# Kernel tuning notes

Hardware: AMD Instinct MI355X
Metric: run time of the kernel (lower is better)

The kernel has to match this reference:

```python
import jax, jax.numpy as jnp
import numpy as np

N = 10000      # nodes
E = 320000     # edges (avg degree 32)
IN = 512       # in_channels
OUT = 128      # out_channels
H = 4          # in_head
C1 = 2 * OUT   # per-head hidden channels of conv1 (256)
NEG_SLOPE = 0.2


def setup_inputs() -> dict:
    key = jax.random.key(0)
    ks = jax.random.split(key, 12)
    x = jax.random.normal(ks[0], (N, IN), dtype=jnp.float32)
    edge_index = jax.random.randint(ks[1], (2, E), 0, N, dtype=jnp.int64)
    def glorot(k, shape):
        lim = np.sqrt(6.0 / (shape[0] + shape[-1])).astype(np.float32)
        return jax.random.uniform(k, shape, jnp.float32, -lim, lim)
    # conv1: GATv2Conv(IN -> C1 per head, heads=H)
    Wl1 = glorot(ks[2], (IN, H * C1))
    Wr1 = glorot(ks[3], (IN, H * C1))
    att1 = glorot(ks[4], (H, C1))
    b1 = jnp.zeros((H * C1,), jnp.float32)
    # conv2: GATv2Conv(H*C1 -> OUT, heads=1)
    Wl2 = glorot(ks[5], (H * C1, OUT))
    Wr2 = glorot(ks[6], (H * C1, OUT))
    att2 = glorot(ks[7], (1, OUT))
    b2 = jnp.zeros((OUT,), jnp.float32)
    return {"x": x, "edge_index": edge_index, "Wl1": Wl1, "Wr1": Wr1,
            "att1": att1, "b1": b1, "Wl2": Wl2, "Wr2": Wr2,
            "att2": att2, "b2": b2}


def gatv2_conv(x, src, dst, Wl, Wr, att, b, heads, ch):
    # x: [N, F_in]; src/dst: [E] (message src -> dst, softmax over dst)
    n = x.shape[0]
    xl = (x @ Wl).reshape(n, heads, ch)   # source-side projection
    xr = (x @ Wr).reshape(n, heads, ch)   # target-side projection
    # per-edge GATv2 score: att . LeakyReLU(xl_j + xr_i)   [E, H]
    e = jax.nn.leaky_relu(xl[src] + xr[dst], NEG_SLOPE)    # [E, H, C]
    s = jnp.einsum('ehc,hc->eh', e, att)                   # [E, H]
    # segment softmax over incoming edges of each dst node
    smax = jax.lax.stop_gradient(jax.ops.segment_max(s, dst, num_segments=n))
    ex = jnp.exp(s - smax[dst])
    denom = jax.ops.segment_sum(ex, dst, num_segments=n)
    alpha = ex / denom[dst]                                # [E, H]
    # weighted scatter-add of source messages
    out = jax.ops.segment_sum(alpha[:, :, None] * xl[src], dst, num_segments=n)
    return out.reshape(n, heads * ch) + b                  # concat heads + bias


def reference(x, edge_index, Wl1, Wr1, att1, b1, Wl2, Wr2, att2, b2):
    src, dst = edge_index[0], edge_index[1]
    h = gatv2_conv(x, src, dst, Wl1, Wr1, att1, b1, H, C1)
    h = jax.nn.relu(h)                                     # [N, H*C1]
    out = gatv2_conv(h, src, dst, Wl2, Wr2, att2, b2, 1, OUT)
    return out                                             # [N, OUT]
```

## Files before the change

kernel.cpp:

```cpp
#include <hip/hip_runtime.h>
#include <cfloat>

#define N_NODES 10000
#define N_EDGES 320000
#define IN_F    512
#define F1      1024
#define OUT_F   128
#define NEG     0.2f
#define BUCKET  128

typedef __attribute__((ext_vector_type(8))) short bf16x8;
typedef __attribute__((ext_vector_type(4))) float f32x4;

__device__ __forceinline__ float lrelu(float v) { return fmaxf(v, NEG * v); }

__device__ __forceinline__ unsigned short f2bf(float f) {
    unsigned u = __float_as_uint(f);
    u += 0x7fff + ((u >> 16) & 1);
    return (unsigned short)(u >> 16);
}
__device__ __forceinline__ float bf2f(unsigned short h) {
    return __uint_as_float(((unsigned)h) << 16);
}
__device__ __forceinline__ void u2f2(unsigned u, float& e0, float& e1) {
    e0 = __uint_as_float(u << 16);
    e1 = __uint_as_float(u & 0xffff0000u);
}

__device__ __forceinline__ float rsum16(float x) {
    x += __int_as_float(__builtin_amdgcn_update_dpp(0, __float_as_int(x), 0x121, 0xF, 0xF, false));
    x += __int_as_float(__builtin_amdgcn_update_dpp(0, __float_as_int(x), 0x122, 0xF, 0xF, false));
    x += __int_as_float(__builtin_amdgcn_update_dpp(0, __float_as_int(x), 0x124, 0xF, 0xF, false));
    x += __int_as_float(__builtin_amdgcn_update_dpp(0, __float_as_int(x), 0x128, 0xF, 0xF, false));
    return x;
}

__device__ __forceinline__ void gld_lds16(const void* g, void* l) {
    __builtin_amdgcn_global_load_lds(
        (const __attribute__((address_space(1))) unsigned int*)g,
        (__attribute__((address_space(3))) unsigned int*)l, 16, 0, 0);
}

#define PB_X  2500
#define PB_S  3750
#define PB_W1 4774
#define PB_END 5030

__device__ __forceinline__ void wt_body(const float* __restrict__ Wa,
                                        const float* __restrict__ Wb,
                                        unsigned short* __restrict__ tbf,
                                        int K, int NS, int n0, int k0, int t,
                                        float (*tile)[33]) {
    int j = t & 31;
    const float* W = (n0 < NS) ? Wa : Wb;
    int nb = (n0 < NS) ? n0 : n0 - NS;
#pragma unroll
    for (int r = 0; r < 4; ++r) {
        int kl = (t >> 5) + r * 8;
        tile[kl][j] = W[(size_t)(k0 + kl) * NS + nb + j];
    }
    __syncthreads();
#pragma unroll
    for (int r = 0; r < 4; ++r) {
        int nl = (t >> 5) + r * 8;
        tbf[(size_t)(n0 + nl) * K + k0 + j] = f2bf(tile[j][nl]);
    }
}

__global__ __launch_bounds__(256) void k_prep(const float* __restrict__ x,
                                              unsigned short* __restrict__ xbf,
                                              const int* __restrict__ ei,
                                              int* __restrict__ cnt,
                                              int* __restrict__ esrc,
                                              const float* __restrict__ Wl1,
                                              const float* __restrict__ Wr1,
                                              unsigned short* __restrict__ w1bf,
                                              const float* __restrict__ Wl2,
                                              const float* __restrict__ Wr2,
                                              unsigned short* __restrict__ w2bf) {
    __shared__ float tile[32][33];
    int bid = blockIdx.x, t = threadIdx.x;
    if (bid < PB_X) {
        int i = bid * 2048 + t * 8;
        float4 v0 = *(const float4*)(x + i);
        float4 v1 = *(const float4*)(x + i + 4);
        ushort4 h0, h1;
        h0.x = f2bf(v0.x); h0.y = f2bf(v0.y); h0.z = f2bf(v0.z); h0.w = f2bf(v0.w);
        h1.x = f2bf(v1.x); h1.y = f2bf(v1.y); h1.z = f2bf(v1.z); h1.w = f2bf(v1.w);
        *(ushort4*)(xbf + i) = h0;
        *(ushort4*)(xbf + i + 4) = h1;
    } else if (bid < PB_S) {
        int e = (bid - PB_X) * 256 + t;
        if (e < N_EDGES) {
            int d = ei[N_EDGES + e];
            int pos = atomicAdd(&cnt[d], 1);
            if (pos < BUCKET) esrc[(size_t)d * BUCKET + pos] = ei[e];
        }
    } else if (bid < PB_W1) {
        int local = bid - PB_S;
        wt_body(Wl1, Wr1, w1bf, IN_F, F1, (local & 63) * 32, (local >> 6) * 32, t, tile);
    } else {
        int local = bid - PB_W1;
        wt_body(Wl2, Wr2, w2bf, F1, OUT_F, (local & 7) * 32, (local >> 3) * 32, t, tile);
    }
}

template<int BM, int WR, int WC>
__global__ __launch_bounds__(256) void gemm_mfma(
        const unsigned short* __restrict__ A,
        const unsigned short* __restrict__ B,
        unsigned short* __restrict__ Cl, unsigned short* __restrict__ Cr,
        int M, int K, int NSPLIT) {
    constexpr int NI = BM / (16 * WR);
    constexpr int NJ = 128 / (16 * WC);
    __shared__ __align__(16) short As[BM * 32];
    __shared__ __align__(16) short Bs[128 * 32];
    int t = threadIdx.x;
    int lane = t & 63, w = t >> 6;
    int row0 = blockIdx.y * BM;
    int n0 = blockIdx.x * 128;
    int wr0 = (w / WC) * (NI * 16);
    int wc0 = (w % WC) * (NJ * 16);
    int q = lane >> 4, md = lane & 15;
    int srow = t >> 2;
    int skoff = (t & 3) * 8;

    f32x4 acc[NI][NJ];
#pragma unroll
    for (int i = 0; i < NI; ++i)
#pragma unroll
        for (int j = 0; j < NJ; ++j)
#pragma unroll
            for (int r = 0; r < 4; ++r) acc[i][j][r] = 0.f;

    for (int k0 = 0; k0 < K; k0 += 32) {
        __syncthreads();
#pragma unroll
        for (int is = 0; is < BM / 64; ++is) {
            int gr = row0 + is * 64 + srow;
            if (gr < M)
                gld_lds16(A + (size_t)gr * K + k0 + skoff,
                          &As[(is * 64 + (t >> 6) * 16) * 32]);
        }
#pragma unroll
        for (int is = 0; is < 2; ++is) {
            int gn = n0 + is * 64 + srow;
            gld_lds16(B + (size_t)gn * K + k0 + skoff,
                      &Bs[(is * 64 + (t >> 6) * 16) * 32]);
        }
        __syncthreads();

        bf16x8 av[NI], bv[NJ];
#pragma unroll
        for (int i = 0; i < NI; ++i)
            av[i] = *(const bf16x8*)&As[(wr0 + i * 16 + md) * 32 + q * 8];
#pragma unroll
        for (int j = 0; j < NJ; ++j)
            bv[j] = *(const bf16x8*)&Bs[(wc0 + j * 16 + md) * 32 + q * 8];
#pragma unroll
        for (int i = 0; i < NI; ++i)
#pragma unroll
            for (int j = 0; j < NJ; ++j)
                acc[i][j] = __builtin_amdgcn_mfma_f32_16x16x32_bf16(av[i], bv[j], acc[i][j], 0, 0, 0);
    }

#pragma unroll
    for (int i = 0; i < NI; ++i)
#pragma unroll
        for (int j = 0; j < NJ; ++j) {
            int col = n0 + wc0 + j * 16 + md;
            unsigned short* C = (col < NSPLIT) ? Cl : Cr;
            int cc = (col < NSPLIT) ? col : col - NSPLIT;
#pragma unroll
            for (int r = 0; r < 4; ++r) {
                int grow = row0 + wr0 + i * 16 + q * 4 + r;
                if (grow < M) C[(size_t)grow * NSPLIT + cc] = f2bf(acc[i][j][r]);
            }
        }
}

__global__ __launch_bounds__(256) void k_pq1(const unsigned short* __restrict__ xlbf,
                                             const float* __restrict__ att,
                                             float* __restrict__ P) {
    int t = threadIdx.x;
    int w = t >> 6, lane = t & 63;
    int nd = blockIdx.x * 4 + w;
    int head = lane >> 4, sub = lane & 15;
    int ch = head * 256 + sub * 16;
    const uint4* px = (const uint4*)(xlbf + (size_t)nd * F1 + ch);
    uint4 xa = px[0], xb = px[1];
    const float4* pa = (const float4*)(att + ch);
    float4 a0 = pa[0], a1 = pa[1], a2 = pa[2], a3 = pa[3];
    float4 c0, c1, c2, c3;
    u2f2(xa.x, c0.x, c0.y); u2f2(xa.y, c0.z, c0.w);
    u2f2(xa.z, c1.x, c1.y); u2f2(xa.w, c1.z, c1.w);
    u2f2(xb.x, c2.x, c2.y); u2f2(xb.y, c2.z, c2.w);
    u2f2(xb.z, c3.x, c3.y); u2f2(xb.w, c3.z, c3.w);
    float s0 = a0.x * c0.x;
    s0 = fmaf(a0.y, c0.y, s0); s0 = fmaf(a0.z, c0.z, s0); s0 = fmaf(a0.w, c0.w, s0);
    float s1 = a1.x * c1.x;
    s1 = fmaf(a1.y, c1.y, s1); s1 = fmaf(a1.z, c1.z, s1); s1 = fmaf(a1.w, c1.w, s1);
    float s2 = a2.x * c2.x;
    s2 = fmaf(a2.y, c2.y, s2); s2 = fmaf(a2.z, c2.z, s2); s2 = fmaf(a2.w, c2.w, s2);
    float s3 = a3.x * c3.x;
    s3 = fmaf(a3.y, c3.y, s3); s3 = fmaf(a3.z, c3.z, s3); s3 = fmaf(a3.w, c3.w, s3);
    float s = rsum16((s0 + s1) + (s2 + s3));
    if (sub == 0) P[nd * 4 + head] = s;
}

__global__ __launch_bounds__(256) void k_fused1(const unsigned short* __restrict__ xlbf,
                                                const unsigned short* __restrict__ xrbf,
                                                const int* __restrict__ cnt,
                                                const int* __restrict__ esrc,
                                                const float* __restrict__ att,
                                                const float* __restrict__ Pbuf,
                                                const float* __restrict__ bias,
                                                unsigned short* __restrict__ hb) {
    int t = threadIdx.x;
    int w = t >> 6, lane = t & 63;
    int nd = blockIdx.x * 4 + w;
    int head = lane >> 4, sub = lane & 15;
    int ch = head * 256 + sub * 16;

    float4 r0, r1, r2, r3;
    {
        const uint4* prx = (const uint4*)(xrbf + (size_t)nd * F1 + ch);
        uint4 xa = prx[0], xb = prx[1];
        u2f2(xa.x, r0.x, r0.y); u2f2(xa.y, r0.z, r0.w);
        u2f2(xa.z, r1.x, r1.y); u2f2(xa.w, r1.z, r1.w);
        u2f2(xb.x, r2.x, r2.y); u2f2(xb.y, r2.z, r2.w);
        u2f2(xb.z, r3.x, r3.y); u2f2(xb.w, r3.z, r3.w);
    }
    const float4* pa = (const float4*)(att + ch);
    float4 a0 = pa[0], a1 = pa[1], a2 = pa[2], a3 = pa[3];

    float qd = a0.x * r0.x;
    qd = fmaf(a0.y, r0.y, qd); qd = fmaf(a0.z, r0.z, qd); qd = fmaf(a0.w, r0.w, qd);
    qd = fmaf(a1.x, r1.x, qd); qd = fmaf(a1.y, r1.y, qd);
    qd = fmaf(a1.z, r1.z, qd); qd = fmaf(a1.w, r1.w, qd);
    qd = fmaf(a2.x, r2.x, qd); qd = fmaf(a2.y, r2.y, qd);
    qd = fmaf(a2.z, r2.z, qd); qd = fmaf(a2.w, r2.w, qd);
    qd = fmaf(a3.x, r3.x, qd); qd = fmaf(a3.y, r3.y, qd);
    qd = fmaf(a3.z, r3.z, qd); qd = fmaf(a3.w, r3.w, qd);
    float Qk = 0.6f * rsum16(qd);

    int deg = min(cnt[nd], BUCKET);
    int p0 = nd * BUCKET;
    int p1 = p0 + deg;

    float l = 0.f;
    float4 acc0 = make_float4(0.f, 0.f, 0.f, 0.f);
    float4 acc1 = acc0, acc2 = acc0, acc3 = acc0;

    uint4 A0 = {}, B0 = {}, A1 = {}, B1 = {};
    float Pv0 = 0.f, Pv1 = 0.f;
    if (p0 < p1) {
        int sn = esrc[p0];
        const uint4* pv = (const uint4*)(xlbf + (size_t)sn * F1 + ch);
        A0 = pv[0]; B0 = pv[1]; Pv0 = Pbuf[sn * 4 + head];
    }
    if (p0 + 1 < p1) {
        int sn = esrc[p0 + 1];
        const uint4* pv = (const uint4*)(xlbf + (size_t)sn * F1 + ch);
        A1 = pv[0]; B1 = pv[1]; Pv1 = Pbuf[sn * 4 + head];
    }
    for (int p = p0; p < p1; ++p) {
        uint4 ca = A0, cb = B0;
        float Pv = Pv0;
        A0 = A1; B0 = B1; Pv0 = Pv1;
        if (p + 2 < p1) {
            int sn = esrc[p + 2];
            const uint4* pv = (const uint4*)(xlbf + (size_t)sn * F1 + ch);
            A1 = pv[0]; B1 = pv[1]; Pv1 = Pbuf[sn * 4 + head];
        }
        float4 c0, c1, c2, c3;
        u2f2(ca.x, c0.x, c0.y); u2f2(ca.y, c0.z, c0.w);
        u2f2(ca.z, c1.x, c1.y); u2f2(ca.w, c1.z, c1.w);
        u2f2(cb.x, c2.x, c2.y); u2f2(cb.y, c2.z, c2.w);
        u2f2(cb.z, c3.x, c3.y); u2f2(cb.w, c3.z, c3.w);
        float s0 = a0.x * fabsf(c0.x + r0.x);
        s0 = fmaf(a0.y, fabsf(c0.y + r0.y), s0);
        s0 = fmaf(a0.z, fabsf(c0.z + r0.z), s0);
        s0 = fmaf(a0.w, fabsf(c0.w + r0.w), s0);
        float s1 = a1.x * fabsf(c1.x + r1.x);
        s1 = fmaf(a1.y, fabsf(c1.y + r1.y), s1);
        s1 = fmaf(a1.z, fabsf(c1.z + r1.z), s1);
        s1 = fmaf(a1.w, fabsf(c1.w + r1.w), s1);
        float s2 = a2.x * fabsf(c2.x + r2.x);
        s2 = fmaf(a2.y, fabsf(c2.y + r2.y), s2);
        s2 = fmaf(a2.z, fabsf(c2.z + r2.z), s2);
        s2 = fmaf(a2.w, fabsf(c2.w + r2.w), s2);
        float s3 = a3.x * fabsf(c3.x + r3.x);
        s3 = fmaf(a3.y, fabsf(c3.y + r3.y), s3);
        s3 = fmaf(a3.z, fabsf(c3.z + r3.z), s3);
        s3 = fmaf(a3.w, fabsf(c3.w + r3.w), s3);
        float sab = rsum16((s0 + s1) + (s2 + s3));
        float sarg = fmaf(0.6f, Pv, Qk);
        sarg = fmaf(0.4f, sab, sarg);
        sarg = fminf(fmaxf(sarg, -60.f), 60.f);
        float al = __expf(sarg);
        l += al;
        acc0.x = fmaf(al, c0.x, acc0.x);
        acc0.y = fmaf(al, c0.y, acc0.y);
        acc0.z = fmaf(al, c0.z, acc0.z);
        acc0.w = fmaf(al, c0.w, acc0.w);
        acc1.x = fmaf(al, c1.x, acc1.x);
        acc1.y = fmaf(al, c1.y, acc1.y);
        acc1.z = fmaf(al, c1.z, acc1.z);
        acc1.w = fmaf(al, c1.w, acc1.w);
        acc2.x = fmaf(al, c2.x, acc2.x);
        acc2.y = fmaf(al, c2.y, acc2.y);
        acc2.z = fmaf(al, c2.z, acc2.z);
        acc2.w = fmaf(al, c2.w, acc2.w);
        acc3.x = fmaf(al, c3.x, acc3.x);
        acc3.y = fmaf(al, c3.y, acc3.y);
        acc3.z = fmaf(al, c3.z, acc3.z);
        acc3.w = fmaf(al, c3.w, acc3.w);
    }

    float invL = (l > 0.f) ? 1.f / l : 0.f;
    const float4* pb = (const float4*)(bias + ch);
    size_t base = (size_t)nd * F1 + ch;
    float4 aa[4] = {acc0, acc1, acc2, acc3};
#pragma unroll
    for (int j = 0; j < 4; ++j) {
        float4 b4 = pb[j];
        ushort4 hv;
        hv.x = f2bf(fmaxf(fmaf(aa[j].x, invL, b4.x), 0.f));
        hv.y = f2bf(fmaxf(fmaf(aa[j].y, invL, b4.y), 0.f));
        hv.z = f2bf(fmaxf(fmaf(aa[j].z, invL, b4.z), 0.f));
        hv.w = f2bf(fmaxf(fmaf(aa[j].w, invL, b4.w), 0.f));
        *(ushort4*)(hb + base + j * 4) = hv;
    }
}

__global__ __launch_bounds__(256) void k_fused2(const unsigned short* __restrict__ xlbf,
                                                const unsigned short* __restrict__ xrbf,
                                                const int* __restrict__ cnt,
                                                const int* __restrict__ esrc,
                                                const float* __restrict__ att,
                                                const float* __restrict__ bias,
                                                float* __restrict__ out) {
    int t = threadIdx.x;
    int w = t >> 6, lane = t & 63;
    int nd = blockIdx.x * 4 + w;
    int g = lane >> 4, sub = lane & 15;
    int ch = sub * 8;

    __shared__ float slx2[4][4];
    __shared__ float sacc2[4][4][132];

    float r[8], a[8];
    {
        uint4 u = *(const uint4*)(xrbf + (size_t)nd * OUT_F + ch);
        u2f2(u.x, r[0], r[1]); u2f2(u.y, r[2], r[3]);
        u2f2(u.z, r[4], r[5]); u2f2(u.w, r[6], r[7]);
        float4 q0 = *(const float4*)(att + ch);
        float4 q1 = *(const float4*)(att + ch + 4);
        a[0] = q0.x; a[1] = q0.y; a[2] = q0.z; a[3] = q0.w;
        a[4] = q1.x; a[5] = q1.y; a[6] = q1.z; a[7] = q1.w;
    }
    int deg = min(cnt[nd], BUCKET);
    int p0 = nd * BUCKET;
    int p1 = p0 + deg;

    float l = 0.f;
    float acc[8] = {};
    uint4 cur, nxt;
    {
        int p = p0 + g;
        if (p < p1)     cur = *(const uint4*)(xlbf + (size_t)esrc[p] * OUT_F + ch);
        if (p + 4 < p1) nxt = *(const uint4*)(xlbf + (size_t)esrc[p + 4] * OUT_F + ch);
    }
    for (int p = p0 + g; p < p1; p += 4) {
        uint4 c = cur;
        cur = nxt;
        if (p + 8 < p1) nxt = *(const uint4*)(xlbf + (size_t)esrc[p + 8] * OUT_F + ch);
        float v[8];
        u2f2(c.x, v[0], v[1]); u2f2(c.y, v[2], v[3]);
        u2f2(c.z, v[4], v[5]); u2f2(c.w, v[6], v[7]);
        float sx = a[0] * lrelu(v[0] + r[0]);
        sx = fmaf(a[1], lrelu(v[1] + r[1]), sx);
        sx = fmaf(a[2], lrelu(v[2] + r[2]), sx);
        sx = fmaf(a[3], lrelu(v[3] + r[3]), sx);
        float sy = a[4] * lrelu(v[4] + r[4]);
        sy = fmaf(a[5], lrelu(v[5] + r[5]), sy);
        sy = fmaf(a[6], lrelu(v[6] + r[6]), sy);
        sy = fmaf(a[7], lrelu(v[7] + r[7]), sy);
        float s = rsum16(sx + sy);
        s = fminf(fmaxf(s, -60.f), 60.f);
        float al = __expf(s);
        l += al;
#pragma unroll
        for (int k = 0; k < 8; ++k) acc[k] = fmaf(al, v[k], acc[k]);
    }

    if (sub == 0) slx2[w][g] = l;
    float4 v0 = make_float4(acc[0], acc[1], acc[2], acc[3]);
    float4 v1 = make_float4(acc[4], acc[5], acc[6], acc[7]);
    *(float4*)&sacc2[w][g][ch] = v0;
    *(float4*)&sacc2[w][g][ch + 4] = v1;
    __syncthreads();
    float L = slx2[w][0] + slx2[w][1] + slx2[w][2] + slx2[w][3];
    float invL = (L > 0.f) ? 1.f / L : 0.f;
    int c2 = lane * 2;
    float o0 = sacc2[w][0][c2] + sacc2[w][1][c2] + sacc2[w][2][c2] + sacc2[w][3][c2];
    float o1 = sacc2[w][0][c2 + 1] + sacc2[w][1][c2 + 1] + sacc2[w][2][c2 + 1] + sacc2[w][3][c2 + 1];
    float2 bf = *(const float2*)(bias + c2);
    float2 o;
    o.x = fmaf(o0, invL, bf.x);
    o.y = fmaf(o1, invL, bf.y);
    *(float2*)(out + (size_t)nd * OUT_F + c2) = o;
}

extern "C" void kernel_launch(void* const* d_in, const int* in_sizes, int n_in,
                              void* d_out, int out_size, void* d_ws, size_t ws_size,
                              hipStream_t stream) {
    const float* x    = (const float*)d_in[0];
    const int*   ei   = (const int*)d_in[1];
    const float* Wl1  = (const float*)d_in[2];
    const float* Wr1  = (const float*)d_in[3];
    const float* att1 = (const float*)d_in[4];
    const float* b1   = (const float*)d_in[5];
    const float* Wl2  = (const float*)d_in[6];
    const float* Wr2  = (const float*)d_in[7];
    const float* att2 = (const float*)d_in[8];
    const float* b2   = (const float*)d_in[9];
    float* out = (float*)d_out;

    unsigned short* us = (unsigned short*)d_ws;
    unsigned short* xl1bf = us;
    unsigned short* xr1bf = xl1bf + (size_t)N_NODES * F1;
    unsigned short* xl2bf = xr1bf + (size_t)N_NODES * F1;
    unsigned short* xr2bf = xl2bf + (size_t)N_NODES * OUT_F;
    unsigned short* hb   = xr2bf + (size_t)N_NODES * OUT_F;
    unsigned short* xbf  = hb + (size_t)N_NODES * F1;
    unsigned short* w1bf = xbf + (size_t)N_NODES * IN_F;
    unsigned short* w2bf = w1bf + (size_t)2048 * IN_F;
    int* cnt   = (int*)(w2bf + (size_t)256 * F1);
    int* esrc  = cnt + (N_NODES + 16);
    float* Pbuf = (float*)(esrc + (size_t)N_NODES * BUCKET);

    hipMemsetAsync(cnt, 0, sizeof(int) * N_NODES, stream);
    k_prep<<<PB_END, 256, 0, stream>>>(x, xbf, ei, cnt, esrc,
                                       Wl1, Wr1, w1bf,
                                       Wl2, Wr2, w2bf);

    gemm_mfma<128, 2, 2><<<dim3(16, (N_NODES + 127) / 128), 256, 0, stream>>>(
        xbf, w1bf, xl1bf, xr1bf, N_NODES, IN_F, F1);

    k_pq1<<<N_NODES / 4, 256, 0, stream>>>(xl1bf, att1, Pbuf);

    k_fused1<<<N_NODES / 4, 256, 0, stream>>>(xl1bf, xr1bf, cnt, esrc, att1, Pbuf, b1, hb);

    gemm_mfma<64, 1, 4><<<dim3(2, (N_NODES + 63) / 64), 256, 0, stream>>>(
        hb, w2bf, xl2bf, xr2bf, N_NODES, F1, OUT_F);

    k_fused2<<<N_NODES / 4, 256, 0, stream>>>(xl2bf, xr2bf, cnt, esrc, att2, b2, out);
}
```

Before: 278.3 us.

## Split each node's edges across four waves with shared-memory reduction in layer-1 aggregation

The layer-1 fused attention/aggregation kernel now assigns one node per block and partitions that node's incoming edges across the block's four waves. Each wave computes partial softmax denominators and weighted accumulators, which are combined through shared memory before wave 0 applies normalization, bias, ReLU and writes bf16 output. This shortens the per-wave serial edge loop to expose more memory-level parallelism. In exchange it adds a block barrier, LDS traffic, redundant per-wave loads of the target features, and idle waves during the epilogue.

New measurement: 276.8 us. Within noise of the previous version (-0.5%).

```diff
diff --git a/kernel.cpp b/kernel.cpp
--- a/kernel.cpp
+++ b/kernel.cpp
@@ -218,9 +218,12 @@
                                                 unsigned short* __restrict__ hb) {
     int t = threadIdx.x;
     int w = t >> 6, lane = t & 63;
-    int nd = blockIdx.x * 4 + w;
+    int nd = blockIdx.x;
     int head = lane >> 4, sub = lane & 15;
     int ch = head * 256 + sub * 16;
+
+    __shared__ float slx[4][4];
+    __shared__ float4 sacc[3][4][64];
 
     float4 r0, r1, r2, r3;
     {
@@ -246,7 +249,9 @@
 
     int deg = min(cnt[nd], BUCKET);
     int p0 = nd * BUCKET;
-    int p1 = p0 + deg;
+    int per = (deg + 3) >> 2;
+    int pa_ = p0 + min(w * per, deg);
+    int pb_ = p0 + min((w + 1) * per, deg);
 
     float l = 0.f;
     float4 acc0 = make_float4(0.f, 0.f, 0.f, 0.f);
@@ -254,21 +259,21 @@
 
     uint4 A0 = {}, B0 = {}, A1 = {}, B1 = {};
     float Pv0 = 0.f, Pv1 = 0.f;
-    if (p0 < p1) {
-        int sn = esrc[p0];
+    if (pa_ < pb_) {
+        int sn = esrc[pa_];
         const uint4* pv = (const uint4*)(xlbf + (size_t)sn * F1 + ch);
         A0 = pv[0]; B0 = pv[1]; Pv0 = Pbuf[sn * 4 + head];
     }
-    if (p0 + 1 < p1) {
-        int sn = esrc[p0 + 1];
+    if (pa_ + 1 < pb_) {
+        int sn = esrc[pa_ + 1];
         const uint4* pv = (const uint4*)(xlbf + (size_t)sn * F1 + ch);
         A1 = pv[0]; B1 = pv[1]; Pv1 = Pbuf[sn * 4 + head];
     }
-    for (int p = p0; p < p1; ++p) {
+    for (int p = pa_; p < pb_; ++p) {
         uint4 ca = A0, cb = B0;
         float Pv = Pv0;
         A0 = A1; B0 = B1; Pv0 = Pv1;
-        if (p + 2 < p1) {
+        if (p + 2 < pb_) {
             int sn = esrc[p + 2];
             const uint4* pv = (const uint4*)(xlbf + (size_t)sn * F1 + ch);
             A1 = pv[0]; B1 = pv[1]; Pv1 = Pbuf[sn * 4 + head];
@@ -318,19 +323,37 @@
         acc3.w = fmaf(al, c3.w, acc3.w);
     }
 
-    float invL = (l > 0.f) ? 1.f / l : 0.f;
-    const float4* pb = (const float4*)(bias + ch);
-    size_t base = (size_t)nd * F1 + ch;
-    float4 aa[4] = {acc0, acc1, acc2, acc3};
-#pragma unroll
-    for (int j = 0; j < 4; ++j) {
-        float4 b4 = pb[j];
-        ushort4 hv;
-        hv.x = f2bf(fmaxf(fmaf(aa[j].x, invL, b4.x), 0.f));
-        hv.y = f2bf(fmaxf(fmaf(aa[j].y, invL, b4.y), 0.f));
-        hv.z = f2bf(fmaxf(fmaf(aa[j].z, invL, b4.z), 0.f));
-        hv.w = f2bf(fmaxf(fmaf(aa[j].w, invL, b4.w), 0.f));
-        *(ushort4*)(hb + base + j * 4) = hv;
+    if (sub == 0) slx[w][head] = l;
+    if (w) {
+        sacc[w - 1][0][lane] = acc0;
+        sacc[w - 1][1][lane] = acc1;
+        sacc[w - 1][2][lane] = acc2;
+        sacc[w - 1][3][lane] = acc3;
+    }
+    __syncthreads();
+    if (w == 0) {
+        float L = slx[0][head] + slx[1][head] + slx[2][head] + slx[3][head];
+        float invL = (L > 0.f) ? 1.f / L : 0.f;
+        const float4* pb = (const float4*)(bias + ch);
+        size_t base = (size_t)nd * F1 + ch;
+        float4 aa[4] = {acc0, acc1, acc2, acc3};
+#pragma unroll
+        for (int j = 0; j < 4; ++j) {
+            float4 q1 = sacc[0][j][lane];
+            float4 q2 = sacc[1][j][lane];
+            float4 q3 = sacc[2][j][lane];
+            float4 b4 = pb[j];
+            float sx = aa[j].x + q1.x + q2.x + q3.x;
+            float sy = aa[j].y + q1.y + q2.y + q3.y;
+            float sz = aa[j].z + q1.z + q2.z + q3.z;
+            float sw = aa[j].w + q1.w + q2.w + q3.w;
+            ushort4 hv;
+            hv.x = f2bf(fmaxf(fmaf(sx, invL, b4.x), 0.f));
+            hv.y = f2bf(fmaxf(fmaf(sy, invL, b4.y), 0.f));
+            hv.z = f2bf(fmaxf(fmaf(sz, invL, b4.z), 0.f));
+            hv.w = f2bf(fmaxf(fmaf(sw, invL, b4.w), 0.f));
+            *(ushort4*)(hb + base + j * 4) = hv;
+        }
     }
 }
 
@@ -451,7 +474,7 @@
 
     k_pq1<<<N_NODES / 4, 256, 0, stream>>>(xl1bf, att1, Pbuf);
 
-    k_fused1<<<N_NODES / 4, 256, 0, stream>>>(xl1bf, xr1bf, cnt, esrc, att1, Pbuf, b1, hb);
+    k_fused1<<<N_NODES, 256, 0, stream>>>(xl1bf, xr1bf, cnt, esrc, att1, Pbuf, b1, hb);
 
     gemm_mfma<64, 1, 4><<<dim3(2, (N_NODES + 63) / 64), 256, 0, stream>>>(
         hb, w2bf, xl2bf, xr2bf, N_NODES, F1, OUT_F);
```

## Split each node's edge list across two wavefronts and deepen gather prefetch

Applied to the files above, without the earlier changes.

The layer-1 aggregation kernel now gives each destination node two wavefronts, each processing half of its incoming edges. Partial softmax denominators and accumulators are combined through shared memory before the bias, ReLU and bf16 store. The gather prefetch grows from two edges in flight to a four-deep register queue, so more memory loads are outstanding. This targets latency-bound gathers, at the cost of twice the blocks, a block-wide barrier and extra register pressure from the queue.

Measured after the change: 280.5 us. Within noise of the previous version (+0.8%).

```diff
diff --git a/kernel.cpp b/kernel.cpp
--- a/kernel.cpp
+++ b/kernel.cpp
@@ -218,9 +218,14 @@
                                                 unsigned short* __restrict__ hb) {
     int t = threadIdx.x;
     int w = t >> 6, lane = t & 63;
-    int nd = blockIdx.x * 4 + w;
+    int ni = w >> 1;
+    int ww = w & 1;
+    int nd = blockIdx.x * 2 + ni;
     int head = lane >> 4, sub = lane & 15;
     int ch = head * 256 + sub * 16;
+
+    __shared__ float slx[4][4];
+    __shared__ float4 sacc4[2][4][64];
 
     float4 r0, r1, r2, r3;
     {
@@ -246,91 +251,111 @@
 
     int deg = min(cnt[nd], BUCKET);
     int p0 = nd * BUCKET;
-    int p1 = p0 + deg;
+    int half = (deg + 1) >> 1;
+    int pa_ = p0 + (ww ? half : 0);
+    int pb_ = p0 + (ww ? deg : half);
 
     float l = 0.f;
     float4 acc0 = make_float4(0.f, 0.f, 0.f, 0.f);
     float4 acc1 = acc0, acc2 = acc0, acc3 = acc0;
 
-    uint4 A0 = {}, B0 = {}, A1 = {}, B1 = {};
-    float Pv0 = 0.f, Pv1 = 0.f;
-    if (p0 < p1) {
-        int sn = esrc[p0];
-        const uint4* pv = (const uint4*)(xlbf + (size_t)sn * F1 + ch);
-        A0 = pv[0]; B0 = pv[1]; Pv0 = Pbuf[sn * 4 + head];
-    }
-    if (p0 + 1 < p1) {
-        int sn = esrc[p0 + 1];
-        const uint4* pv = (const uint4*)(xlbf + (size_t)sn * F1 + ch);
-        A1 = pv[0]; B1 = pv[1]; Pv1 = Pbuf[sn * 4 + head];
-    }
-    for (int p = p0; p < p1; ++p) {
-        uint4 ca = A0, cb = B0;
-        float Pv = Pv0;
-        A0 = A1; B0 = B1; Pv0 = Pv1;
-        if (p + 2 < p1) {
-            int sn = esrc[p + 2];
+    uint4 Aq[4], Bq[4];
+    float Pq[4];
+#pragma unroll
+    for (int k = 0; k < 4; ++k) {
+        Aq[k] = make_uint4(0, 0, 0, 0);
+        Bq[k] = make_uint4(0, 0, 0, 0);
+        Pq[k] = 0.f;
+        int pp = pa_ + k;
+        if (pp < pb_) {
+            int sn = esrc[pp];
             const uint4* pv = (const uint4*)(xlbf + (size_t)sn * F1 + ch);
-            A1 = pv[0]; B1 = pv[1]; Pv1 = Pbuf[sn * 4 + head];
-        }
-        float4 c0, c1, c2, c3;
-        u2f2(ca.x, c0.x, c0.y); u2f2(ca.y, c0.z, c0.w);
-        u2f2(ca.z, c1.x, c1.y); u2f2(ca.w, c1.z, c1.w);
-        u2f2(cb.x, c2.x, c2.y); u2f2(cb.y, c2.z, c2.w);
-        u2f2(cb.z, c3.x, c3.y); u2f2(cb.w, c3.z, c3.w);
-        float s0 = a0.x * fabsf(c0.x + r0.x);
-        s0 = fmaf(a0.y, fabsf(c0.y + r0.y), s0);
-        s0 = fmaf(a0.z, fabsf(c0.z + r0.z), s0);
-        s0 = fmaf(a0.w, fabsf(c0.w + r0.w), s0);
-        float s1 = a1.x * fabsf(c1.x + r1.x);
-        s1 = fmaf(a1.y, fabsf(c1.y + r1.y), s1);
-        s1 = fmaf(a1.z, fabsf(c1.z + r1.z), s1);
-        s1 = fmaf(a1.w, fabsf(c1.w + r1.w), s1);
-        float s2 = a2.x * fabsf(c2.x + r2.x);
-        s2 = fmaf(a2.y, fabsf(c2.y + r2.y), s2);
-        s2 = fmaf(a2.z, fabsf(c2.z + r2.z), s2);
-        s2 = fmaf(a2.w, fabsf(c2.w + r2.w), s2);
-        float s3 = a3.x * fabsf(c3.x + r3.x);
-        s3 = fmaf(a3.y, fabsf(c3.y + r3.y), s3);
-        s3 = fmaf(a3.z, fabsf(c3.z + r3.z), s3);
-        s3 = fmaf(a3.w, fabsf(c3.w + r3.w), s3);
-        float sab = rsum16((s0 + s1) + (s2 + s3));
-        float sarg = fmaf(0.6f, Pv, Qk);
-        sarg = fmaf(0.4f, sab, sarg);
-        sarg = fminf(fmaxf(sarg, -60.f), 60.f);
-        float al = __expf(sarg);
-        l += al;
-        acc0.x = fmaf(al, c0.x, acc0.x);
-        acc0.y = fmaf(al, c0.y, acc0.y);
-        acc0.z = fmaf(al, c0.z, acc0.z);
-        acc0.w = fmaf(al, c0.w, acc0.w);
-        acc1.x = fmaf(al, c1.x, acc1.x);
-        acc1.y = fmaf(al, c1.y, acc1.y);
-        acc1.z = fmaf(al, c1.z, acc1.z);
-        acc1.w = fmaf(al, c1.w, acc1.w);
-        acc2.x = fmaf(al, c2.x, acc2.x);
-        acc2.y = fmaf(al, c2.y, acc2.y);
-        acc2.z = fmaf(al, c2.z, acc2.z);
-        acc2.w = fmaf(al, c2.w, acc2.w);
-        acc3.x = fmaf(al, c3.x, acc3.x);
-        acc3.y = fmaf(al, c3.y, acc3.y);
-        acc3.z = fmaf(al, c3.z, acc3.z);
-        acc3.w = fmaf(al, c3.w, acc3.w);
-    }
-
-    float invL = (l > 0.f) ? 1.f / l : 0.f;
-    const float4* pb = (const float4*)(bias + ch);
-    size_t base = (size_t)nd * F1 + ch;
-    float4 aa[4] = {acc0, acc1, acc2, acc3};
-#pragma unroll
-    for (int j = 0; j < 4; ++j) {
-        float4 b4 = pb[j];
-        ushort4 hv;
-        hv.x = f2bf(fmaxf(fmaf(aa[j].x, invL, b4.x), 0.f));
-        hv.y = f2bf(fmaxf(fmaf(aa[j].y, invL, b4.y), 0.f));
-        hv.z = f2bf(fmaxf(fmaf(aa[j].z, invL, b4.z), 0.f));
-        hv.w = f2bf(fmaxf(fmaf(aa[j].w, invL, b4.w), 0.f));
-        *(ushort4*)(hb + base + j * 4) = hv;
+            Aq[k] = pv[0]; Bq[k] = pv[1]; Pq[k] = Pbuf[sn * 4 + head];
+        }
+    }
+    for (int p = pa_; p < pb_; p += 4) {
+#pragma unroll
+        for (int k = 0; k < 4; ++k) {
+            if (p + k < pb_) {
+                uint4 ca = Aq[k], cb = Bq[k];
+                float Pv = Pq[k];
+                if (p + k + 4 < pb_) {
+                    int sn = esrc[p + k + 4];
+                    const uint4* pv = (const uint4*)(xlbf + (size_t)sn * F1 + ch);
+                    Aq[k] = pv[0]; Bq[k] = pv[1]; Pq[k] = Pbuf[sn * 4 + head];
+                }
+                float4 c0, c1, c2, c3;
+                u2f2(ca.x, c0.x, c0.y); u2f2(ca.y, c0.z, c0.w);
+                u2f2(ca.z, c1.x, c1.y); u2f2(ca.w, c1.z, c1.w);
+                u2f2(cb.x, c2.x, c2.y); u2f2(cb.y, c2.z, c2.w);
+                u2f2(cb.z, c3.x, c3.y); u2f2(cb.w, c3.z, c3.w);
+                float s0 = a0.x * fabsf(c0.x + r0.x);
+                s0 = fmaf(a0.y, fabsf(c0.y + r0.y), s0);
+                s0 = fmaf(a0.z, fabsf(c0.z + r0.z), s0);
+                s0 = fmaf(a0.w, fabsf(c0.w + r0.w), s0);
+                float s1 = a1.x * fabsf(c1.x + r1.x);
+                s1 = fmaf(a1.y, fabsf(c1.y + r1.y), s1);
+                s1 = fmaf(a1.z, fabsf(c1.z + r1.z), s1);
+                s1 = fmaf(a1.w, fabsf(c1.w + r1.w), s1);
+                float s2 = a2.x * fabsf(c2.x + r2.x);
+                s2 = fmaf(a2.y, fabsf(c2.y + r2.y), s2);
+                s2 = fmaf(a2.z, fabsf(c2.z + r2.z), s2);
+                s2 = fmaf(a2.w, fabsf(c2.w + r2.w), s2);
+                float s3 = a3.x * fabsf(c3.x + r3.x);
+                s3 = fmaf(a3.y, fabsf(c3.y + r3.y), s3);
+                s3 = fmaf(a3.z, fabsf(c3.z + r3.z), s3);
+                s3 = fmaf(a3.w, fabsf(c3.w + r3.w), s3);
+                float sab = rsum16((s0 + s1) + (s2 + s3));
+                float sarg = fmaf(0.6f, Pv, Qk);
+                sarg = fmaf(0.4f, sab, sarg);
+                sarg = fminf(fmaxf(sarg, -60.f), 60.f);
+                float al = __expf(sarg);
+                l += al;
+                acc0.x = fmaf(al, c0.x, acc0.x);
+                acc0.y = fmaf(al, c0.y, acc0.y);
+                acc0.z = fmaf(al, c0.z, acc0.z);
+                acc0.w = fmaf(al, c0.w, acc0.w);
+                acc1.x = fmaf(al, c1.x, acc1.x);
+                acc1.y = fmaf(al, c1.y, acc1.y);
+                acc1.z = fmaf(al, c1.z, acc1.z);
+                acc1.w = fmaf(al, c1.w, acc1.w);
+                acc2.x = fmaf(al, c2.x, acc2.x);
+                acc2.y = fmaf(al, c2.y, acc2.y);
+                acc2.z = fmaf(al, c2.z, acc2.z);
+                acc2.w = fmaf(al, c2.w, acc2.w);
+                acc3.x = fmaf(al, c3.x, acc3.x);
+                acc3.y = fmaf(al, c3.y, acc3.y);
+                acc3.z = fmaf(al, c3.z, acc3.z);
+                acc3.w = fmaf(al, c3.w, acc3.w);
+            }
+        }
+    }
+
+    if (sub == 0) slx[w][head] = l;
+    if (ww == 1) {
+        sacc4[ni][0][lane] = acc0;
+        sacc4[ni][1][lane] = acc1;
+        sacc4[ni][2][lane] = acc2;
+        sacc4[ni][3][lane] = acc3;
+    }
+    __syncthreads();
+    if (ww == 0) {
+        float L = l + slx[w ^ 1][head];
+        float invL = (L > 0.f) ? 1.f / L : 0.f;
+        const float4* pb = (const float4*)(bias + ch);
+        size_t base = (size_t)nd * F1 + ch;
+        float4 aa[4] = {acc0, acc1, acc2, acc3};
+#pragma unroll
+        for (int j = 0; j < 4; ++j) {
+            float4 pt = sacc4[ni][j][lane];
+            float4 b4 = pb[j];
+            ushort4 hv;
+            hv.x = f2bf(fmaxf(fmaf(aa[j].x + pt.x, invL, b4.x), 0.f));
+            hv.y = f2bf(fmaxf(fmaf(aa[j].y + pt.y, invL, b4.y), 0.f));
+            hv.z = f2bf(fmaxf(fmaf(aa[j].z + pt.z, invL, b4.z), 0.f));
+            hv.w = f2bf(fmaxf(fmaf(aa[j].w + pt.w, invL, b4.w), 0.f));
+            *(ushort4*)(hb + base + j * 4) = hv;
+        }
     }
 }
 
@@ -451,7 +476,7 @@
 
     k_pq1<<<N_NODES / 4, 256, 0, stream>>>(xl1bf, att1, Pbuf);
 
-    k_fused1<<<N_NODES / 4, 256, 0, stream>>>(xl1bf, xr1bf, cnt, esrc, att1, Pbuf, b1, hb);
+    k_fused1<<<N_NODES / 2, 256, 0, stream>>>(xl1bf, xr1bf, cnt, esrc, att1, Pbuf, b1, hb);
 
     gemm_mfma<64, 1, 4><<<dim3(2, (N_NODES + 63) / 64), 256, 0, stream>>>(
         hb, w2bf, xl2bf, xr2bf, N_NODES, F1, OUT_F);
```
